# Optimization experiments

Measured on AMD Instinct MI355X. Metric: run time of the kernel, lower is better.

Reference implementation:

```python
import jax, jax.numpy as jnp
import numpy as np

B, L, D, N = 16, 512, 768, 8192


def setup_inputs() -> dict:
    key = jax.random.key(0)
    k = jax.random.split(key, 5)
    return {
        "y": jax.random.normal(k[0], (B, L, D), dtype=jnp.float32),
        "Wy_w": jax.random.normal(k[1], (D, D), dtype=jnp.float32) * 0.02,
        "Wy_b": jnp.zeros((D,), dtype=jnp.float32),
        "Wz_w": jax.random.normal(k[2], (D, D), dtype=jnp.float32) * 0.02,
        "Wz_b": jnp.zeros((D,), dtype=jnp.float32),
        "dic_z": jax.random.normal(k[3], (N, D), dtype=jnp.float32),
        "prior": jax.random.uniform(k[4], (N,), dtype=jnp.float32),
    }


def reference(y, Wy_w, Wy_b, Wz_w, Wz_b, dic_z, prior):
    # y: [B,L,D]; dic_z: [N,D]; prior: [N]
    d = y.shape[-1]
    qy = jnp.einsum('bld,ed->ble', y, Wy_w) + Wy_b          # Wy(y): [B,L,D]
    kz = jnp.einsum('nd,ed->ne', dic_z, Wz_w) + Wz_b        # Wz(dic_z): [N,D]
    scores = jnp.einsum('bld,nd->bln', qy, kz) / jnp.sqrt(jnp.float32(d))
    attn = jax.nn.softmax(scores, axis=-1)                   # [B,L,N]
    # z[b,l,d] = sum_n prior[n] * attn[b,l,n] * dic_z[n,d]
    # == (attn * prior) @ dic_z, avoiding the [L,N,D] intermediate.
    z = jnp.einsum('bln,nd->bld', attn * prior, dic_z)       # [B,L,D]
    return z
```

## Files before the change

kernel.cpp:

```cpp
#include <hip/hip_runtime.h>
#include <stdint.h>

#define M_ 8192
#define D_ 768
#define N_ 8192

typedef unsigned short u16;
typedef __attribute__((ext_vector_type(8))) unsigned short us8;
typedef __attribute__((ext_vector_type(8))) __bf16 bf16x8;
typedef __attribute__((ext_vector_type(4))) float f32x4;

__device__ __forceinline__ u16 f2bf(float f) {
  uint32_t u = __builtin_bit_cast(uint32_t, f);
  u += 0x7FFFu + ((u >> 16) & 1u);
  return (u16)(u >> 16);
}

__device__ __forceinline__ void gload_lds16(const void* g, void* l) {
  __builtin_amdgcn_global_load_lds(
      (__attribute__((address_space(1))) void*)g,
      (__attribute__((address_space(3))) void*)l, 16, 0, 0);
}

__global__ __launch_bounds__(256)
void k_cvt2(const float* __restrict__ a, const float* __restrict__ b,
            u16* __restrict__ da, u16* __restrict__ db, int n4each) {
  int stride = gridDim.x * blockDim.x;
  for (int i = blockIdx.x * blockDim.x + threadIdx.x; i < 2 * n4each; i += stride) {
    const float* s = (i < n4each) ? a : b;
    u16* d = (i < n4each) ? da : db;
    int j = (i < n4each) ? i : i - n4each;
    float4 v = reinterpret_cast<const float4*>(s)[j];
    ushort4 o;
    o.x = f2bf(v.x); o.y = f2bf(v.y); o.z = f2bf(v.z); o.w = f2bf(v.w);
    reinterpret_cast<ushort4*>(d)[j] = o;
  }
}

__global__ __launch_bounds__(256)
void k_build_vt(const float* __restrict__ dic, const float* __restrict__ prior,
                u16* __restrict__ Vt) {
  __shared__ float t[32][33];
  const int n0 = blockIdx.x * 32, d0 = blockIdx.y * 32;
  const int tx = threadIdx.x, ty = threadIdx.y;
  #pragma unroll
  for (int i = ty; i < 32; i += 8)
    t[i][tx] = dic[(size_t)(n0 + i) * D_ + d0 + tx] * prior[n0 + i];
  __syncthreads();
  #pragma unroll
  for (int i = ty; i < 32; i += 8)
    Vt[(size_t)(d0 + i) * N_ + n0 + tx] = f2bf(t[tx][i]);
}

__global__ __launch_bounds__(512, 2)
void k_gemm8(const u16* __restrict__ A, const u16* __restrict__ Bm,
             u16* __restrict__ Cb, float* __restrict__ Cf, float scale,
             long ldk, int K, int Ncols, int nbx) {
  extern __shared__ u16 ldsu[];
  const int tid = threadIdx.x;
  const int lane = tid & 63, wid = tid >> 6;
  const int wr = wid >> 2, wc = wid & 3;
  const int L15 = lane & 15, L7 = lane & 7, g = lane >> 4;

  const int nwg = gridDim.x;
  const int bid = blockIdx.x;
  const int wg = ((nwg & 7) == 0) ? ((bid & 7) * (nwg >> 3) + (bid >> 3)) : bid;
  const int bx = wg % nbx, by = wg / nbx;
  const long m0 = (long)by * 256;
  const long n0 = (long)bx * 256;
  const int NT = K >> 6;

  int aBase[2], bBase[2];
  #pragma unroll
  for (int ks = 0; ks < 2; ++ks) {
    const int slot = (((ks * 4 + g) ^ L7) << 3);
    aBase[ks] = wr * 8192 + L15 * 64 + slot;
    bBase[ks] = 16384 + (wc >> 1) * 8192 + (wc & 1) * 4096 + L15 * 64 + slot;
  }

  const int rowoff = wid * 8 + (lane >> 3);
  const int colsw = ((lane & 7) ^ (lane >> 3)) << 3;
  const u16* Ag = A + m0 * ldk;
  const u16* Bg = Bm + n0 * ldk;
  u16* ldsW = ldsu + tid * 8;

  auto g1 = [&](int t, int mat, int r0) {
    if (t >= NT) return;
    const u16* src = (mat ? Bg : Ag) + (size_t)(r0 + rowoff) * ldk
                     + (size_t)t * 64 + colsw;
    gload_lds16(src, ldsW + (t & 1) * 32768 + mat * 16384 + (r0 >> 6) * 512 * 8);
  };

#define RD_B()                                                              \
  _Pragma("unroll") for (int j = 0; j < 4; ++j)                             \
    _Pragma("unroll") for (int ks = 0; ks < 2; ++ks)                        \
      bfr[j][ks] = __builtin_bit_cast(bf16x8,                               \
          *reinterpret_cast<const us8*>(&ldsu[bufOff + bBase[ks] + j * 1024]));
#define RD_A(q)                                                             \
  _Pragma("unroll") for (int t = 0; t < 2; ++t)                             \
    _Pragma("unroll") for (int ks = 0; ks < 2; ++ks)                        \
      afr[t][ks] = __builtin_bit_cast(bf16x8,                               \
          *reinterpret_cast<const us8*>(                                    \
              &ldsu[bufOff + aBase[ks] + (2 * (q) + t) * 1024]));
#define LGKM0()                                                             \
  asm volatile("s_waitcnt lgkmcnt(0)" ::: "memory");                        \
  __builtin_amdgcn_sched_barrier(0);
#define MM(p)                                                               \
  __builtin_amdgcn_s_setprio(1);                                            \
  _Pragma("unroll") for (int ks = 0; ks < 2; ++ks)                          \
    _Pragma("unroll") for (int t = 0; t < 2; ++t)                           \
      _Pragma("unroll") for (int j = 0; j < 4; ++j)                         \
        acc[2 * (p) + t][j] = __builtin_amdgcn_mfma_f32_16x16x32_bf16(      \
            afr[t][ks], bfr[j][ks], acc[2 * (p) + t][j], 0, 0, 0);          \
  __builtin_amdgcn_s_setprio(0);

  g1(0, 1, 0); g1(0, 1, 64); g1(0, 1, 128); g1(0, 1, 192);
  g1(0, 0, 0); g1(0, 0, 128); g1(0, 0, 64); g1(0, 0, 192);
  g1(1, 1, 0); g1(1, 1, 64);
  g1(1, 1, 128); g1(1, 1, 192);
  g1(1, 0, 0); g1(1, 0, 128);
  asm volatile("s_waitcnt vmcnt(6)" ::: "memory");
  __builtin_amdgcn_s_barrier();

  f32x4 acc[8][4] = {};

  for (int k = 0; k < NT; ++k) {
    const int bufOff = (k & 1) * 32768;
    bf16x8 bfr[4][2];

    { bf16x8 afr[2][2];
      g1(k + 1, 0, 64); g1(k + 1, 0, 192);
      RD_B(); RD_A(0);
      asm volatile("s_waitcnt lgkmcnt(8)" ::: "memory");
      __builtin_amdgcn_s_barrier();
      LGKM0(); MM(0);
    }
    { bf16x8 afr[2][2];
      RD_A(1);
      g1(k + 2, 1, 0); g1(k + 2, 1, 64);
      __builtin_amdgcn_s_barrier();
      LGKM0(); MM(1);
    }
    { bf16x8 afr[2][2];
      RD_A(2);
      g1(k + 2, 1, 128); g1(k + 2, 1, 192);
      __builtin_amdgcn_s_barrier();
      LGKM0(); MM(2);
    }
    { bf16x8 afr[2][2];
      RD_A(3);
      g1(k + 2, 0, 0); g1(k + 2, 0, 128);
      if (k < NT - 2) asm volatile("s_waitcnt vmcnt(6)" ::: "memory");
      else            asm volatile("s_waitcnt vmcnt(0)" ::: "memory");
      __builtin_amdgcn_s_barrier();
      LGKM0(); MM(3);
    }
  }
#undef RD_B
#undef RD_A
#undef LGKM0
#undef MM

  __builtin_amdgcn_s_barrier();
  float* lsum = reinterpret_cast<float*>(ldsu);
  #pragma unroll
  for (int i = 0; i < 8; ++i) {
    #pragma unroll
    for (int q = 0; q < 4; ++q) {
      const int rl = wr * 128 + i * 16 + g * 4 + q;
      const long row = m0 + rl;
      float rsum = 0.f;
      #pragma unroll
      for (int j = 0; j < 4; ++j) {
        float v = __expf(acc[i][j][q] * scale);
        rsum += v;
        Cb[row * (long)Ncols + n0 + wc * 64 + j * 16 + L15] = f2bf(v);
      }
      lsum[rl * 68 + wc * 16 + L15] = rsum;
    }
  }
  __builtin_amdgcn_s_barrier();
  {
    const int rl = tid >> 1, half = tid & 1;
    const float4* rp =
        reinterpret_cast<const float4*>(&lsum[rl * 68 + half * 32]);
    float s4 = 0.f;
    #pragma unroll
    for (int c = 0; c < 8; ++c) {
      float4 v = rp[c];
      s4 += (v.x + v.y) + (v.z + v.w);
    }
    s4 += __shfl_xor(s4, 1);
    if (half == 0) atomicAdd(&Cf[m0 + rl], s4);
  }
}

__global__ __launch_bounds__(256, 2)
void k_pv128(const u16* __restrict__ A, const u16* __restrict__ Bm,
             const float* __restrict__ rowsum, float* __restrict__ out,
             int nbx, long ldk, int K) {
  extern __shared__ u16 ldsu[];
  const int tid = threadIdx.x;
  const int lane = tid & 63, wid = tid >> 6;
  const int wr = wid >> 1, wc = wid & 1;
  const int L15 = lane & 15, L7 = lane & 7, g = lane >> 4;

  const int nwg = gridDim.x, bid = blockIdx.x;
  const int wg = ((nwg & 7) == 0) ? ((bid & 7) * (nwg >> 3) + (bid >> 3)) : bid;
  const int bx = wg % nbx, by = wg / nbx;
  const long m0 = (long)by * 128, n0 = (long)bx * 128;
  const int NT = K >> 6;

  int aBase[2], bBase[2];
  #pragma unroll
  for (int ks = 0; ks < 2; ++ks) {
    const int slot = (((ks * 4 + g) ^ L7) << 3);
    aBase[ks] = (wr * 64 + L15) * 64 + slot;
    bBase[ks] = 8192 + (wc * 64 + L15) * 64 + slot;
  }

  const int rowoff = tid >> 3;
  const int colsw = ((tid & 7) ^ ((tid >> 3) & 7)) << 3;
  const u16* Ag = A + m0 * ldk;
  const u16* Bg = Bm + n0 * ldk;
  u16* ldsW = ldsu + tid * 8;

  auto g1 = [&](int t, int mat, int r0) {
    if (t >= NT) return;
    const u16* src = (mat ? Bg : Ag) + (size_t)(r0 + rowoff) * ldk
                     + (size_t)t * 64 + colsw;
    gload_lds16(src, ldsW + (t & 1) * 16384 + mat * 8192 + r0 * 64);
  };

#define PLGKM0()                                                            \
  asm volatile("s_waitcnt lgkmcnt(0)" ::: "memory");                        \
  __builtin_amdgcn_sched_barrier(0);
#define PMM(p)                                                              \
  __builtin_amdgcn_s_setprio(1);                                            \
  _Pragma("unroll") for (int ks = 0; ks < 2; ++ks)                          \
    _Pragma("unroll") for (int j = 0; j < 4; ++j)                           \
      acc[p][j] = __builtin_amdgcn_mfma_f32_16x16x32_bf16(                  \
          afr[ks], bfr[j][ks], acc[p][j], 0, 0, 0);                         \
  __builtin_amdgcn_s_setprio(0);
#define PRD_A(q)                                                            \
  _Pragma("unroll") for (int ks = 0; ks < 2; ++ks)                          \
    afr[ks] = __builtin_bit_cast(bf16x8,                                    \
        *reinterpret_cast<const us8*>(&ldsu[bufOff + aBase[ks] + (q) * 1024]));

  g1(0, 1, 0); g1(0, 1, 32); g1(0, 1, 64); g1(0, 1, 96);
  g1(0, 0, 0); g1(0, 0, 32); g1(0, 0, 64); g1(0, 0, 96);
  g1(1, 1, 0); g1(1, 1, 32); g1(1, 1, 64); g1(1, 1, 96);
  g1(1, 0, 0); g1(1, 0, 32);
  asm volatile("s_waitcnt vmcnt(6)" ::: "memory");
  __builtin_amdgcn_s_barrier();

  f32x4 acc[4][4] = {};

  for (int k = 0; k < NT; ++k) {
    const int bufOff = (k & 1) * 16384;
    bf16x8 bfr[4][2];

    { bf16x8 afr[2];
      g1(k + 1, 0, 64); g1(k + 1, 0, 96);
      #pragma unroll
      for (int j = 0; j < 4; ++j)
        #pragma unroll
        for (int ks = 0; ks < 2; ++ks)
          bfr[j][ks] = __builtin_bit_cast(bf16x8,
              *reinterpret_cast<const us8*>(&ldsu[bufOff + bBase[ks] + j * 1024]));
      PRD_A(0);
      asm volatile("s_waitcnt lgkmcnt(8)" ::: "memory");
      __builtin_amdgcn_s_barrier();
      PLGKM0(); PMM(0);
    }
    { bf16x8 afr[2];
      PRD_A(1);
      g1(k + 2, 1, 0); g1(k + 2, 1, 32);
      __builtin_amdgcn_s_barrier();
      PLGKM0(); PMM(1);
    }
    { bf16x8 afr[2];
      PRD_A(2);
      g1(k + 2, 1, 64); g1(k + 2, 1, 96);
      __builtin_amdgcn_s_barrier();
      PLGKM0(); PMM(2);
    }
    { bf16x8 afr[2];
      PRD_A(3);
      g1(k + 2, 0, 0); g1(k + 2, 0, 32);
      if (k < NT - 2) asm volatile("s_waitcnt vmcnt(6)" ::: "memory");
      else            asm volatile("s_waitcnt vmcnt(0)" ::: "memory");
      __builtin_amdgcn_s_barrier();
      PLGKM0(); PMM(3);
    }
  }
#undef PLGKM0
#undef PMM
#undef PRD_A

  #pragma unroll
  for (int i = 0; i < 4; ++i) {
    #pragma unroll
    for (int q = 0; q < 4; ++q) {
      long row = m0 + wr * 64 + i * 16 + g * 4 + q;
      float inv = 1.0f / rowsum[row];
      #pragma unroll
      for (int j = 0; j < 4; ++j) {
        long col = n0 + wc * 64 + j * 16 + L15;
        out[row * D_ + col] = acc[i][j][q] * inv;
      }
    }
  }
}

__global__ __launch_bounds__(256, 2)
void k_projf(const float* __restrict__ Af, const u16* __restrict__ Bm,
             u16* __restrict__ Cb, const float* __restrict__ bias, long K) {
  __shared__ u16 Al[128 * 64];
  __shared__ u16 Bl[128 * 64];
  const int tid = threadIdx.x;
  const int lane = tid & 63;
  const int wave = tid >> 6;
  const int wr = wave >> 1, wc = wave & 1;
  const int L15 = lane & 15, L7 = lane & 7, g = lane >> 4;
  const long m0 = (long)blockIdx.y * 128;
  const long n0 = (long)blockIdx.x * 128;

  f32x4 acc[4][4] = {};

  const int arow = tid >> 3;
  const int acol = (tid & 7) * 8;
  const int aswz = ((tid & 7) ^ ((tid >> 3) & 7)) * 8;
  const u16* gB = Bm + (n0 + (tid >> 3)) * K + aswz;

  for (long kt = 0; kt < K; kt += 64) {
    __syncthreads();
    #pragma unroll
    for (int r = 0; r < 4; ++r) {
      const float* src = Af + (m0 + r * 32 + arow) * K + kt + acol;
      float4 v0 = *reinterpret_cast<const float4*>(src);
      float4 v1 = *reinterpret_cast<const float4*>(src + 4);
      us8 o;
      o[0] = f2bf(v0.x); o[1] = f2bf(v0.y); o[2] = f2bf(v0.z); o[3] = f2bf(v0.w);
      o[4] = f2bf(v1.x); o[5] = f2bf(v1.y); o[6] = f2bf(v1.z); o[7] = f2bf(v1.w);
      *reinterpret_cast<us8*>(&Al[(r * 32 + arow) * 64 + aswz]) = o;
      gload_lds16(gB + (size_t)(r * 32) * K + kt, &Bl[r * 2048 + tid * 8]);
    }
    __syncthreads();
    #pragma unroll
    for (int ks = 0; ks < 2; ++ks) {
      const int slot = ((ks * 4 + g) ^ L7) * 8;
      bf16x8 av[4], bv[4];
      #pragma unroll
      for (int i = 0; i < 4; ++i) {
        av[i] = __builtin_bit_cast(bf16x8, *reinterpret_cast<const us8*>(
            &Al[(wr * 64 + i * 16 + L15) * 64 + slot]));
        bv[i] = __builtin_bit_cast(bf16x8, *reinterpret_cast<const us8*>(
            &Bl[(wc * 64 + i * 16 + L15) * 64 + slot]));
      }
      #pragma unroll
      for (int i = 0; i < 4; ++i)
        #pragma unroll
        for (int j = 0; j < 4; ++j)
          acc[i][j] = __builtin_amdgcn_mfma_f32_16x16x32_bf16(av[i], bv[j], acc[i][j], 0, 0, 0);
    }
  }

  #pragma unroll
  for (int i = 0; i < 4; ++i)
    #pragma unroll
    for (int q = 0; q < 4; ++q) {
      long row = m0 + wr * 64 + i * 16 + g * 4 + q;
      #pragma unroll
      for (int j = 0; j < 4; ++j) {
        long col = n0 + wc * 64 + j * 16 + L15;
        Cb[row * D_ + col] = f2bf(acc[i][j][q] + bias[col]);
      }
    }
}

extern "C" void kernel_launch(void* const* d_in, const int* in_sizes, int n_in,
                              void* d_out, int out_size, void* d_ws, size_t ws_size,
                              hipStream_t stream) {
  (void)in_sizes; (void)n_in; (void)out_size;
  const float* y     = (const float*)d_in[0];
  const float* Wy_w  = (const float*)d_in[1];
  const float* Wy_b  = (const float*)d_in[2];
  const float* Wz_w  = (const float*)d_in[3];
  const float* Wz_b  = (const float*)d_in[4];
  const float* dic   = (const float*)d_in[5];
  const float* prior = (const float*)d_in[6];
  float* out = (float*)d_out;

  hipFuncSetAttribute(reinterpret_cast<const void*>(&k_gemm8),
                      hipFuncAttributeMaxDynamicSharedMemorySize, 131072);
  hipFuncSetAttribute(reinterpret_cast<const void*>(&k_pv128),
                      hipFuncAttributeMaxDynamicSharedMemorySize, 65536);

  char* base = (char*)d_ws;
  size_t off = 0;
  auto alloc = [&](size_t bytes) -> char* {
    char* p = base + off;
    off = (off + bytes + 255) & ~(size_t)255;
    return p;
  };
  u16*  Wyb  = (u16*)alloc((size_t)D_ * D_ * 2);
  u16*  Wzb  = (u16*)alloc((size_t)D_ * D_ * 2);
  u16*  Qb   = (u16*)alloc((size_t)M_ * D_ * 2);
  u16*  Kb   = (u16*)alloc((size_t)N_ * D_ * 2);
  u16*  Vt   = (u16*)alloc((size_t)D_ * N_ * 2);
  float* rowsum = (float*)alloc((size_t)M_ * 4);
  size_t fixed = off;
  int Mc = M_;
  while (Mc > 256 && fixed + (size_t)Mc * N_ * 2 > ws_size) Mc >>= 1;
  u16* Sc = (u16*)alloc((size_t)Mc * N_ * 2);

  hipMemsetAsync(rowsum, 0, (size_t)M_ * 4, stream);

  {
    int n4e = D_ * D_ / 4;
    int blocks = (2 * n4e + 255) / 256;
    if (blocks > 2048) blocks = 2048;
    hipLaunchKernelGGL(k_cvt2, dim3(blocks), dim3(256), 0, stream,
                       Wy_w, Wz_w, Wyb, Wzb, n4e);
  }

  hipLaunchKernelGGL(k_build_vt, dim3(N_ / 32, D_ / 32), dim3(32, 8), 0, stream,
                     dic, prior, Vt);

  hipLaunchKernelGGL(k_projf, dim3(D_ / 128, M_ / 128), dim3(256), 0, stream,
                     y, Wyb, Qb, Wy_b, (long)D_);
  hipLaunchKernelGGL(k_projf, dim3(D_ / 128, N_ / 128), dim3(256), 0, stream,
                     dic, Wzb, Kb, Wz_b, (long)D_);

  const float scale = 0.036084391824351615f;
  for (int mc = 0; mc < M_; mc += Mc) {
    {
      const int nbx = N_ / 256, nby = Mc / 256;
      hipLaunchKernelGGL(k_gemm8, dim3(nbx * nby), dim3(512), 131072, stream,
                         Qb + (size_t)mc * D_, Kb, Sc, rowsum + mc, scale,
                         (long)D_, D_, N_, nbx);
    }
    {
      const int nbx = D_ / 128, nby = Mc / 128;
      hipLaunchKernelGGL(k_pv128, dim3(nbx * nby), dim3(256), 65536, stream,
                         Sc, Vt, rowsum + mc, out + (size_t)mc * D_,
                         nbx, (long)N_, N_);
    }
  }
}
```

Baseline: 304.1 us.

## Pre-convert inputs to bf16 and merge the two projection GEMMs into one launch

Converts y to bf16 in a separate kernel and has k_build_vt also write a bf16 copy of dic_z. The projection kernel then loads both A and B tiles with direct global-to-LDS loads, and the Q and K projections run in a single launch whose grid covers both. This removes the in-loop fp32 load and convert work from the GEMM and fills the GPU better with one combined grid. The cost is an extra pass over y, an extra bf16 write of dic_z, and more workspace.

```diff
diff --git a/kernel.cpp b/kernel.cpp
--- a/kernel.cpp
+++ b/kernel.cpp
@@ -20,6 +20,17 @@
   __builtin_amdgcn_global_load_lds(
       (__attribute__((address_space(1))) void*)g,
       (__attribute__((address_space(3))) void*)l, 16, 0, 0);
+}
+
+__global__ __launch_bounds__(256)
+void k_cvt_bf16(const float* __restrict__ in, u16* __restrict__ out, int n4) {
+  int stride = gridDim.x * blockDim.x;
+  for (int i = blockIdx.x * blockDim.x + threadIdx.x; i < n4; i += stride) {
+    float4 v = reinterpret_cast<const float4*>(in)[i];
+    ushort4 o;
+    o.x = f2bf(v.x); o.y = f2bf(v.y); o.z = f2bf(v.z); o.w = f2bf(v.w);
+    reinterpret_cast<ushort4*>(out)[i] = o;
+  }
 }
 
 __global__ __launch_bounds__(256)
@@ -39,13 +50,16 @@
 
 __global__ __launch_bounds__(256)
 void k_build_vt(const float* __restrict__ dic, const float* __restrict__ prior,
-                u16* __restrict__ Vt) {
+                u16* __restrict__ Db, u16* __restrict__ Vt) {
   __shared__ float t[32][33];
   const int n0 = blockIdx.x * 32, d0 = blockIdx.y * 32;
   const int tx = threadIdx.x, ty = threadIdx.y;
   #pragma unroll
-  for (int i = ty; i < 32; i += 8)
-    t[i][tx] = dic[(size_t)(n0 + i) * D_ + d0 + tx] * prior[n0 + i];
+  for (int i = ty; i < 32; i += 8) {
+    float v = dic[(size_t)(n0 + i) * D_ + d0 + tx];
+    Db[(size_t)(n0 + i) * D_ + d0 + tx] = f2bf(v);
+    t[i][tx] = v * prior[n0 + i];
+  }
   __syncthreads();
   #pragma unroll
   for (int i = ty; i < 32; i += 8)
@@ -314,8 +328,11 @@
 }
 
 __global__ __launch_bounds__(256, 2)
-void k_projf(const float* __restrict__ Af, const u16* __restrict__ Bm,
-             u16* __restrict__ Cb, const float* __restrict__ bias, long K) {
+void k_proj(const u16* __restrict__ A0, const u16* __restrict__ A1,
+            const u16* __restrict__ Bm0, const u16* __restrict__ Bm1,
+            u16* __restrict__ C0, u16* __restrict__ C1,
+            const float* __restrict__ b0, const float* __restrict__ b1,
+            int nby0, long K) {
   __shared__ u16 Al[128 * 64];
   __shared__ u16 Bl[128 * 64];
   const int tid = threadIdx.x;
@@ -323,27 +340,29 @@
   const int wave = tid >> 6;
   const int wr = wave >> 1, wc = wave & 1;
   const int L15 = lane & 15, L7 = lane & 7, g = lane >> 4;
-  const long m0 = (long)blockIdx.y * 128;
+
+  int by = blockIdx.y;
+  const bool second = (by >= nby0);
+  if (second) by -= nby0;
+  const u16* A  = second ? A1 : A0;
+  const u16* Bm = second ? Bm1 : Bm0;
+  u16* Cb       = second ? C1 : C0;
+  const float* bias = second ? b1 : b0;
+
+  const long m0 = (long)by * 128;
   const long n0 = (long)blockIdx.x * 128;
 
   f32x4 acc[4][4] = {};
 
-  const int arow = tid >> 3;
-  const int acol = (tid & 7) * 8;
-  const int aswz = ((tid & 7) ^ ((tid >> 3) & 7)) * 8;
-  const u16* gB = Bm + (n0 + (tid >> 3)) * K + aswz;
+  const int colsw = ((tid & 7) ^ ((tid >> 3) & 7)) * 8;
+  const u16* gA = A + (m0 + (tid >> 3)) * K + colsw;
+  const u16* gB = Bm + (n0 + (tid >> 3)) * K + colsw;
 
   for (long kt = 0; kt < K; kt += 64) {
     __syncthreads();
     #pragma unroll
     for (int r = 0; r < 4; ++r) {
-      const float* src = Af + (m0 + r * 32 + arow) * K + kt + acol;
-      float4 v0 = *reinterpret_cast<const float4*>(src);
-      float4 v1 = *reinterpret_cast<const float4*>(src + 4);
-      us8 o;
-      o[0] = f2bf(v0.x); o[1] = f2bf(v0.y); o[2] = f2bf(v0.z); o[3] = f2bf(v0.w);
-      o[4] = f2bf(v1.x); o[5] = f2bf(v1.y); o[6] = f2bf(v1.z); o[7] = f2bf(v1.w);
-      *reinterpret_cast<us8*>(&Al[(r * 32 + arow) * 64 + aswz]) = o;
+      gload_lds16(gA + (size_t)(r * 32) * K + kt, &Al[r * 2048 + tid * 8]);
       gload_lds16(gB + (size_t)(r * 32) * K + kt, &Bl[r * 2048 + tid * 8]);
     }
     __syncthreads();
@@ -404,6 +423,8 @@
     off = (off + bytes + 255) & ~(size_t)255;
     return p;
   };
+  u16*  Yb   = (u16*)alloc((size_t)M_ * D_ * 2);
+  u16*  Db   = (u16*)alloc((size_t)N_ * D_ * 2);
   u16*  Wyb  = (u16*)alloc((size_t)D_ * D_ * 2);
   u16*  Wzb  = (u16*)alloc((size_t)D_ * D_ * 2);
   u16*  Qb   = (u16*)alloc((size_t)M_ * D_ * 2);
@@ -418,6 +439,12 @@
   hipMemsetAsync(rowsum, 0, (size_t)M_ * 4, stream);
 
   {
+    int n4 = M_ * D_ / 4;
+    int blocks = (n4 + 255) / 256;
+    if (blocks > 2048) blocks = 2048;
+    hipLaunchKernelGGL(k_cvt_bf16, dim3(blocks), dim3(256), 0, stream, y, Yb, n4);
+  }
+  {
     int n4e = D_ * D_ / 4;
     int blocks = (2 * n4e + 255) / 256;
     if (blocks > 2048) blocks = 2048;
@@ -426,12 +453,10 @@
   }
 
   hipLaunchKernelGGL(k_build_vt, dim3(N_ / 32, D_ / 32), dim3(32, 8), 0, stream,
-                     dic, prior, Vt);
-
-  hipLaunchKernelGGL(k_projf, dim3(D_ / 128, M_ / 128), dim3(256), 0, stream,
-                     y, Wyb, Qb, Wy_b, (long)D_);
-  hipLaunchKernelGGL(k_projf, dim3(D_ / 128, N_ / 128), dim3(256), 0, stream,
-                     dic, Wzb, Kb, Wz_b, (long)D_);
+                     dic, prior, Db, Vt);
+
+  hipLaunchKernelGGL(k_proj, dim3(D_ / 128, M_ / 128 + N_ / 128), dim3(256), 0, stream,
+                     Yb, Db, Wyb, Wzb, Qb, Kb, Wy_b, Wz_b, M_ / 128, (long)D_);
 
   const float scale = 0.036084391824351615f;
   for (int mc = 0; mc < M_; mc += Mc) {
```

New measurement: 287.8 us, median of 2. -5.4%, faster.
